# Kernel optimization log

Hardware: AMD Instinct MI355X
Metric: run time of the kernel (lower is better)

The kernel has to match this reference:

```python
import jax, jax.numpy as jnp
import numpy as np

D_MODEL = 1024
N_HEADS = 16
HEAD_DIM = D_MODEL // N_HEADS
D_FF = 4096
EPS = 1e-5


def layer_norm(x, w, b):
    mu = jnp.mean(x, axis=-1, keepdims=True)
    var = jnp.var(x, axis=-1, keepdims=True)
    return (x - mu) * jax.lax.rsqrt(var + EPS) * w + b


def setup_inputs() -> dict:
    key = jax.random.key(0)
    ks = jax.random.split(key, 8)
    B, T, C = 2, 2048, D_MODEL
    s = lambda fan_in: 1.0 / np.sqrt(fan_in)
    return {
        "x": jax.random.normal(ks[0], (B, T, C), dtype=jnp.float32),
        "ln1_w": jnp.ones((C,), jnp.float32),
        "ln1_b": jnp.zeros((C,), jnp.float32),
        "qkv_w": jax.random.normal(ks[1], (3 * C, C), jnp.float32) * s(C),
        "attn_out_w": jax.random.normal(ks[2], (C, C), jnp.float32) * s(C),
        "ln2_w": jnp.ones((C,), jnp.float32),
        "ln2_b": jnp.zeros((C,), jnp.float32),
        "mlp_in_w": jax.random.normal(ks[3], (D_FF, C), jnp.float32) * s(C),
        "mlp_gate_w": jax.random.normal(ks[4], (D_FF, C), jnp.float32) * s(C),
        "mlp_out_w": jax.random.normal(ks[5], (C, D_FF), jnp.float32) * s(D_FF),
    }


def reference(x, ln1_w, ln1_b, qkv_w, attn_out_w, ln2_w, ln2_b,
              mlp_in_w, mlp_gate_w, mlp_out_w):
    B, T, C = x.shape
    # --- causal self-attention (pre-norm) ---
    h = layer_norm(x, ln1_w, ln1_b)
    qkv = h @ qkv_w.T  # [B,T,3C]
    q, k, v = jnp.split(qkv, 3, axis=-1)
    def heads(t):
        return t.reshape(B, T, N_HEADS, HEAD_DIM).transpose(0, 2, 1, 3)  # [B,H,T,Dh]
    q, k, v = heads(q), heads(k), heads(v)
    scale = HEAD_DIM ** -0.5
    scores = jnp.einsum("bhqd,bhkd->bhqk", q, k) * scale  # [B,H,T,T]
    causal = jnp.tril(jnp.ones((T, T), dtype=bool))
    scores = jnp.where(causal, scores, -jnp.inf)
    attn = jax.nn.softmax(scores, axis=-1)
    out = jnp.einsum("bhqk,bhkd->bhqd", attn, v)
    out = out.transpose(0, 2, 1, 3).reshape(B, T, C)
    x = x + out @ attn_out_w.T
    # --- SwiGLU MLP (pre-norm) ---
    h = layer_norm(x, ln2_w, ln2_b)
    acts = jax.nn.silu(h @ mlp_in_w.T) * (h @ mlp_gate_w.T)
    return x + acts @ mlp_out_w.T
```

## Files before the change

kernel.cpp:

```cpp
#include <hip/hip_runtime.h>
#include <cstdint>

typedef unsigned short u16;
typedef __bf16 bf16x8 __attribute__((ext_vector_type(8)));
typedef float  f32x4  __attribute__((ext_vector_type(4)));

struct alignas(16) F4 { float v[4]; };
struct alignas(8)  U4 { u16 v[4]; };
struct alignas(16) U8 { u16 v[8]; };

__device__ __forceinline__ u16 f2bf(float f) {
    union { float f; unsigned int u; } x; x.f = f;
    unsigned int r = x.u + 0x7fffu + ((x.u >> 16) & 1u);
    return (u16)(r >> 16);
}
__device__ __forceinline__ float bf2f(u16 u) {
    union { unsigned int u; float f; } x; x.u = ((unsigned int)u) << 16;
    return x.f;
}
__device__ __forceinline__ f32x4 mfma16(bf16x8 a, bf16x8 b, f32x4 c) {
    return __builtin_amdgcn_mfma_f32_16x16x32_bf16(a, b, c, 0, 0, 0);
}
__device__ __forceinline__ bf16x8 ldf(const u16* p) { return *(const bf16x8*)p; }
__device__ __forceinline__ void gload_lds16(const void* g, void* l) {
    auto* gp = reinterpret_cast<const __attribute__((address_space(1))) unsigned int*>(
        reinterpret_cast<uintptr_t>(g));
    auto* lp = reinterpret_cast<__attribute__((address_space(3))) unsigned int*>(
        reinterpret_cast<uintptr_t>(l));
    __builtin_amdgcn_global_load_lds(gp, lp, 16, 0, 0);
}

__global__ __launch_bounds__(256) void cast_all_k(const float* __restrict__ qkvw,
                                                  const float* __restrict__ attow,
                                                  const float* __restrict__ mlpow,
                                                  const float* __restrict__ wi,
                                                  const float* __restrict__ wg,
                                                  u16* __restrict__ wq,
                                                  u16* __restrict__ wo,
                                                  u16* __restrict__ wm,
                                                  u16* __restrict__ wig) {
    constexpr int N1 = 3 * 1024 * 1024 / 8;
    constexpr int N2 = N1 + 1024 * 1024 / 8;
    constexpr int N3 = N2 + 1024 * 4096 / 8;
    const int i = blockIdx.x * 256 + threadIdx.x;
    const float* src; u16* dst;
    if (i < N1)      { src = qkvw  + (size_t)i * 8;        dst = wq + (size_t)i * 8; }
    else if (i < N2) { const int j = i - N1; src = attow + (size_t)j * 8; dst = wo + (size_t)j * 8; }
    else if (i < N3) { const int j = i - N2; src = mlpow + (size_t)j * 8; dst = wm + (size_t)j * 8; }
    else {
        const int j = i - N3;
        const int w = j >> 7, c8 = (j & 127) * 8;
        const int f = ((w >> 6) << 5) | (w & 31);
        src = ((w & 32) ? wg : wi) + (size_t)f * 1024 + c8;
        dst = wig + (size_t)w * 1024 + c8;
    }
    F4 a = *(const F4*)src;
    F4 b = *(const F4*)(src + 4);
    U8 o;
    #pragma unroll
    for (int j = 0; j < 4; ++j) { o.v[j] = f2bf(a.v[j]); o.v[4 + j] = f2bf(b.v[j]); }
    *(U8*)dst = o;
}

__global__ __launch_bounds__(256) void ln_fwd_k(const float* __restrict__ x,
                                                const float* __restrict__ w,
                                                const float* __restrict__ b,
                                                u16* __restrict__ h) {
    const int row = blockIdx.x, tid = threadIdx.x;
    const float* xr = x + (size_t)row * 1024;
    F4 v = *(const F4*)(xr + tid * 4);
    float s  = v.v[0] + v.v[1] + v.v[2] + v.v[3];
    float ss = v.v[0]*v.v[0] + v.v[1]*v.v[1] + v.v[2]*v.v[2] + v.v[3]*v.v[3];
    #pragma unroll
    for (int o = 32; o > 0; o >>= 1) { s += __shfl_down(s, o); ss += __shfl_down(ss, o); }
    __shared__ float red[8];
    const int wave = tid >> 6, lane = tid & 63;
    if (lane == 0) { red[wave] = s; red[4 + wave] = ss; }
    __syncthreads();
    s  = red[0] + red[1] + red[2] + red[3];
    ss = red[4] + red[5] + red[6] + red[7];
    const float mu   = s * (1.0f / 1024.0f);
    const float var  = ss * (1.0f / 1024.0f) - mu * mu;
    const float rstd = rsqrtf(var + 1e-5f);
    U4 o;
    #pragma unroll
    for (int j = 0; j < 4; ++j)
        o.v[j] = f2bf((v.v[j] - mu) * rstd * w[tid * 4 + j] + b[tid * 4 + j]);
    *(U4*)(h + (size_t)row * 1024 + tid * 4) = o;
}

__global__ __launch_bounds__(256) void ln_resid_k(const float* __restrict__ x,
                                                  const u16* __restrict__ p,
                                                  const float* __restrict__ w,
                                                  const float* __restrict__ b,
                                                  float* __restrict__ x1,
                                                  u16* __restrict__ h,
                                                  int planeEls) {
    const int row = blockIdx.x, tid = threadIdx.x;
    const size_t base = (size_t)row * 1024 + tid * 4;
    F4 xv = *(const F4*)(x + base);
    U4 q0 = *(const U4*)(p + base);
    U4 q1 = *(const U4*)(p + (size_t)planeEls + base);
    F4 sv;
    #pragma unroll
    for (int j = 0; j < 4; ++j) sv.v[j] = xv.v[j] + bf2f(q0.v[j]) + bf2f(q1.v[j]);
    *(F4*)(x1 + base) = sv;
    float s  = sv.v[0] + sv.v[1] + sv.v[2] + sv.v[3];
    float ss = sv.v[0]*sv.v[0] + sv.v[1]*sv.v[1] + sv.v[2]*sv.v[2] + sv.v[3]*sv.v[3];
    #pragma unroll
    for (int o = 32; o > 0; o >>= 1) { s += __shfl_down(s, o); ss += __shfl_down(ss, o); }
    __shared__ float red[8];
    const int wave = tid >> 6, lane = tid & 63;
    if (lane == 0) { red[wave] = s; red[4 + wave] = ss; }
    __syncthreads();
    s  = red[0] + red[1] + red[2] + red[3];
    ss = red[4] + red[5] + red[6] + red[7];
    const float mu   = s * (1.0f / 1024.0f);
    const float var  = ss * (1.0f / 1024.0f) - mu * mu;
    const float rstd = rsqrtf(var + 1e-5f);
    U4 o;
    #pragma unroll
    for (int j = 0; j < 4; ++j)
        o.v[j] = f2bf((sv.v[j] - mu) * rstd * w[tid * 4 + j] + b[tid * 4 + j]);
    *(U4*)(h + base) = o;
}

__global__ __launch_bounds__(256) void gemm_qkvt_k(const u16* __restrict__ h1,
                                                   const u16* __restrict__ wq,
                                                   u16* __restrict__ qk_b,
                                                   u16* __restrict__ vt_b) {
    __shared__ alignas(16) u16 Alds[128 * 32];
    __shared__ alignas(16) u16 Blds[128 * 32];
    const int tid  = threadIdx.x;
    const int lane = tid & 63, wave = tid >> 6;
    const int wr = wave >> 1, wc = wave & 1;
    const int r16 = lane & 15, g16 = lane >> 4;

    const u16* A; const u16* Bm; u16* Cout; int bn, bm, N;
    const int bid = blockIdx.x;
    if (bid < 512) { A = h1; Bm = wq; Cout = qk_b; N = 2048; bn = bid & 15; bm = bid >> 4; }
    else {
        const int id = bid - 512;
        A = wq + (size_t)2 * 1024 * 1024;
        Bm = h1; Cout = vt_b; N = 4096; bn = id & 31; bm = id >> 5;
    }
    constexpr int K = 1024;

    const int srow = lane >> 2;
    const int scol = (lane & 3) * 8;

    f32x4 acc[4][4] = {};

    for (int k0 = 0; k0 < K; k0 += 32) {
        #pragma unroll
        for (int c = 0; c < 2; ++c) {
            const int ch = wave * 2 + c;
            const u16* ga = A  + ((size_t)bm * 128 + ch * 16 + srow) * K + k0 + scol;
            gload_lds16(ga, &Alds[ch * 512]);
            const u16* gb = Bm + ((size_t)bn * 128 + ch * 16 + srow) * K + k0 + scol;
            gload_lds16(gb, &Blds[ch * 512]);
        }
        __syncthreads();
        bf16x8 af[4], bfr[4];
        #pragma unroll
        for (int m = 0; m < 4; ++m)
            af[m] = ldf(&Alds[(wr * 64 + m * 16 + r16) * 32 + g16 * 8]);
        #pragma unroll
        for (int n = 0; n < 4; ++n)
            bfr[n] = ldf(&Blds[(wc * 64 + n * 16 + r16) * 32 + g16 * 8]);
        #pragma unroll
        for (int m = 0; m < 4; ++m)
            #pragma unroll
            for (int n = 0; n < 4; ++n)
                acc[m][n] = mfma16(af[m], bfr[n], acc[m][n]);
        __syncthreads();
    }

    #pragma unroll
    for (int m = 0; m < 4; ++m)
        #pragma unroll
        for (int n = 0; n < 4; ++n)
            #pragma unroll
            for (int r = 0; r < 4; ++r) {
                const int row = bm * 128 + wr * 64 + m * 16 + g16 * 4 + r;
                const int col = bn * 128 + wc * 64 + n * 16 + r16;
                Cout[(size_t)row * N + col] = f2bf(acc[m][n][r]);
            }
}

__global__ __launch_bounds__(256) void gemm_btsplit_k(const u16* __restrict__ A,
                                                      const u16* __restrict__ Bm,
                                                      u16* __restrict__ P,
                                                      int N, int K, int kchunk,
                                                      int planeEls) {
    __shared__ alignas(16) u16 Alds[128 * 32];
    __shared__ alignas(16) u16 Blds[128 * 32];
    const int tid  = threadIdx.x;
    const int lane = tid & 63, wave = tid >> 6;
    const int wr = wave >> 1, wc = wave & 1;
    const int r16 = lane & 15, g16 = lane >> 4;
    const int bn = blockIdx.x, bm = blockIdx.y;
    const int kBeg = blockIdx.z * kchunk;

    const int srow = lane >> 2;
    const int scol = (lane & 3) * 8;

    f32x4 acc[4][4] = {};

    for (int k0 = kBeg; k0 < kBeg + kchunk; k0 += 32) {
        #pragma unroll
        for (int c = 0; c < 2; ++c) {
            const int ch = wave * 2 + c;
            const u16* ga = A  + ((size_t)bm * 128 + ch * 16 + srow) * K + k0 + scol;
            gload_lds16(ga, &Alds[ch * 512]);
            const u16* gb = Bm + ((size_t)bn * 128 + ch * 16 + srow) * K + k0 + scol;
            gload_lds16(gb, &Blds[ch * 512]);
        }
        __syncthreads();
        bf16x8 af[4], bfr[4];
        #pragma unroll
        for (int m = 0; m < 4; ++m)
            af[m] = ldf(&Alds[(wr * 64 + m * 16 + r16) * 32 + g16 * 8]);
        #pragma unroll
        for (int n = 0; n < 4; ++n)
            bfr[n] = ldf(&Blds[(wc * 64 + n * 16 + r16) * 32 + g16 * 8]);
        #pragma unroll
        for (int m = 0; m < 4; ++m)
            #pragma unroll
            for (int n = 0; n < 4; ++n)
                acc[m][n] = mfma16(af[m], bfr[n], acc[m][n]);
        __syncthreads();
    }

    u16* Pp = P + (size_t)blockIdx.z * planeEls;
    #pragma unroll
    for (int m = 0; m < 4; ++m)
        #pragma unroll
        for (int n = 0; n < 4; ++n)
            #pragma unroll
            for (int r = 0; r < 4; ++r) {
                const int row = bm * 128 + wr * 64 + m * 16 + g16 * 4 + r;
                const int col = bn * 128 + wc * 64 + n * 16 + r16;
                Pp[(size_t)row * N + col] = f2bf(acc[m][n][r]);
            }
}

template <int EPI>
__global__ __launch_bounds__(512, 2)
void gemm256_k(const u16* __restrict__ A, const u16* __restrict__ Bm,
               void* __restrict__ Cout, int lda, int ldb, int kLen,
               int nx, int bnCh, int outLd, int planeEls) {
    __shared__ alignas(16) u16 lds[2][2][2][128 * 64];

    const int tid  = threadIdx.x;
    const int wave = tid >> 6, lane = tid & 63;
    const int wm = wave >> 2, wn = wave & 3;
    const int r16 = lane & 15, g16 = lane >> 4;

    const int cpx = gridDim.x >> 3;
    const int xcd = blockIdx.x & 7, loc = blockIdx.x >> 3;
    const int mCh = cpx / bnCh;
    const int cpr = nx / bnCh;
    const int bm = (xcd / cpr) * mCh + loc / bnCh;
    const int bn = (xcd % cpr) * bnCh + loc % bnCh;
    const int kBeg = blockIdx.z * kLen;
    const int NT = kLen >> 6;

    const int csw = ((lane & 7) ^ (lane >> 3)) * 8;
    const u16* aU = A  + (size_t)(bm * 256) * lda + kBeg;
    const u16* bU = Bm + (size_t)(bn * 256) * ldb + kBeg;
    int aOff[2][2], bOff[2][2];
    #pragma unroll
    for (int h = 0; h < 2; ++h)
        #pragma unroll
        for (int i = 0; i < 2; ++i) {
            const int wr = wave * 16 + (lane >> 3) + i * 8;
            const int ar = (wr >> 6) * 128 + h * 64 + (wr & 63);
            const int br = (wr >> 5) * 64 + h * 32 + (wr & 31);
            aOff[h][i] = ar * lda + csw;
            bOff[h][i] = br * ldb + csw;
        }

    auto stA = [&](int kt, int h) {
        u16* d = &lds[kt & 1][0][h][wave * 1024];
        gload_lds16(aU + aOff[h][0] + kt * 64, d);
        gload_lds16(aU + aOff[h][1] + kt * 64, d + 512);
    };
    auto stB = [&](int kt, int h) {
        u16* d = &lds[kt & 1][1][h][wave * 1024];
        gload_lds16(bU + bOff[h][0] + kt * 64, d);
        gload_lds16(bU + bOff[h][1] + kt * 64, d + 512);
    };

    int offA[4][2], offB[2][2];
    #pragma unroll
    for (int m = 0; m < 4; ++m)
        #pragma unroll
        for (int ks = 0; ks < 2; ++ks)
            offA[m][ks] = (wm * 64 + m * 16 + r16) * 64 + (((ks * 4 + g16) ^ (r16 & 7)) * 8);
    #pragma unroll
    for (int n = 0; n < 2; ++n)
        #pragma unroll
        for (int ks = 0; ks < 2; ++ks)
            offB[n][ks] = (wn * 32 + n * 16 + r16) * 64 + (((ks * 4 + g16) ^ (r16 & 7)) * 8);

    f32x4 acc[8][4] = {};
    bf16x8 af0[4][2], af1[4][2], b0v[2][2], b1v[2][2];

    auto rdAF0 = [&](int buf) {
        const u16* P = &lds[buf][0][0][0];
        #pragma unroll
        for (int m = 0; m < 4; ++m) { af0[m][0] = ldf(P + offA[m][0]); af0[m][1] = ldf(P + offA[m][1]); }
    };
    auto rdAF1 = [&](int buf) {
        const u16* P = &lds[buf][0][1][0];
        #pragma unroll
        for (int m = 0; m < 4; ++m) { af1[m][0] = ldf(P + offA[m][0]); af1[m][1] = ldf(P + offA[m][1]); }
    };
    auto rdB0 = [&](int buf) {
        const u16* P = &lds[buf][1][0][0];
        #pragma unroll
        for (int n = 0; n < 2; ++n) { b0v[n][0] = ldf(P + offB[n][0]); b0v[n][1] = ldf(P + offB[n][1]); }
    };
    auto rdB1 = [&](int buf) {
        const u16* P = &lds[buf][1][1][0];
        #pragma unroll
        for (int n = 0; n < 2; ++n) { b1v[n][0] = ldf(P + offB[n][0]); b1v[n][1] = ldf(P + offB[n][1]); }
    };

    stA(0, 0); stB(0, 0); stB(0, 1); stA(0, 1);
    stA(1, 0); stB(1, 0); stB(1, 1); stA(1, 1);
    asm volatile("s_waitcnt vmcnt(8)" ::: "memory");
    __builtin_amdgcn_s_barrier();
    rdAF0(0); rdB0(0); rdB1(0); rdAF1(0);

    for (int kt = 0; kt < NT; ++kt) {
        const bool pf = (kt + 2 < NT);
        const int nb = (kt + 1) & 1;

        __builtin_amdgcn_s_setprio(1);
        #pragma unroll
        for (int m = 0; m < 4; ++m)
            #pragma unroll
            for (int n = 0; n < 2; ++n) {
                acc[m][n] = mfma16(af0[m][0], b0v[n][0], acc[m][n]);
                acc[m][n] = mfma16(af0[m][1], b0v[n][1], acc[m][n]);
            }
        __builtin_amdgcn_s_setprio(0);
        __builtin_amdgcn_s_barrier();

        if (pf) { stA(kt + 2, 0); stB(kt + 2, 0); }
        __builtin_amdgcn_s_setprio(1);
        #pragma unroll
        for (int m = 0; m < 4; ++m)
            #pragma unroll
            for (int n = 0; n < 2; ++n) {
                acc[m][n + 2] = mfma16(af0[m][0], b1v[n][0], acc[m][n + 2]);
                acc[m][n + 2] = mfma16(af0[m][1], b1v[n][1], acc[m][n + 2]);
            }
        __builtin_amdgcn_s_setprio(0);
        __builtin_amdgcn_s_barrier();

        if (pf) stB(kt + 2, 1);
        __builtin_amdgcn_s_setprio(1);
        #pragma unroll
        for (int m = 0; m < 4; ++m)
            #pragma unroll
            for (int n = 0; n < 2; ++n) {
                acc[m + 4][n] = mfma16(af1[m][0], b0v[n][0], acc[m + 4][n]);
                acc[m + 4][n] = mfma16(af1[m][1], b0v[n][1], acc[m + 4][n]);
            }
        __builtin_amdgcn_s_setprio(0);
        __builtin_amdgcn_s_barrier();

        if (pf) stA(kt + 2, 1);
        if (pf)               { asm volatile("s_waitcnt vmcnt(8)" ::: "memory"); }
        else if (kt + 1 < NT) { asm volatile("s_waitcnt vmcnt(0)" ::: "memory"); }
        if (kt + 1 < NT) {
            __builtin_amdgcn_s_barrier();
            rdAF0(nb); rdB0(nb);
        }
        __builtin_amdgcn_s_setprio(1);
        #pragma unroll
        for (int m = 0; m < 4; ++m)
            #pragma unroll
            for (int n = 0; n < 2; ++n) {
                acc[m + 4][n + 2] = mfma16(af1[m][0], b1v[n][0], acc[m + 4][n + 2]);
                acc[m + 4][n + 2] = mfma16(af1[m][1], b1v[n][1], acc[m + 4][n + 2]);
            }
        __builtin_amdgcn_s_setprio(0);
        if (kt + 1 < NT) { rdB1(nb); rdAF1(nb); }
    }

    if constexpr (EPI == 1) {
        u16* P = (u16*)Cout + (size_t)blockIdx.z * planeEls;
        #pragma unroll
        for (int m = 0; m < 8; ++m)
            #pragma unroll
            for (int n = 0; n < 4; ++n)
                #pragma unroll
                for (int r = 0; r < 4; ++r) {
                    const int row = bm * 256 + wm * 128 + m * 16 + g16 * 4 + r;
                    const int col = bn * 256 + wn * 64 + n * 16 + r16;
                    P[(size_t)row * outLd + col] = f2bf(acc[m][n][r]);
                }
    } else {
        (void)planeEls;
        u16* O = (u16*)Cout;
        #pragma unroll
        for (int m = 0; m < 8; ++m)
            #pragma unroll
            for (int n = 0; n < 2; ++n)
                #pragma unroll
                for (int r = 0; r < 4; ++r) {
                    const int row = bm * 256 + wm * 128 + m * 16 + g16 * 4 + r;
                    const int col = (bn * 4 + wn) * 32 + n * 16 + r16;
                    const float vi = acc[m][n][r];
                    const float vg = acc[m][n + 2][r];
                    const float sl = vi / (1.0f + __expf(-vi));
                    O[(size_t)row * outLd + col] = f2bf(sl * vg);
                }
    }
}

__global__ __launch_bounds__(256) void addreduce4_k(const float* __restrict__ resid,
                                                    const u16* __restrict__ p,
                                                    float* __restrict__ out,
                                                    int n4, int planeEls) {
    for (int i = blockIdx.x * 256 + threadIdx.x; i < n4; i += gridDim.x * 256) {
        F4 a = *(const F4*)(resid + (size_t)i * 4);
        U4 q0 = *(const U4*)(p + (size_t)i * 4);
        U4 q1 = *(const U4*)(p + (size_t)planeEls + (size_t)i * 4);
        U4 q2 = *(const U4*)(p + (size_t)2 * planeEls + (size_t)i * 4);
        U4 q3 = *(const U4*)(p + (size_t)3 * planeEls + (size_t)i * 4);
        F4 o;
        #pragma unroll
        for (int j = 0; j < 4; ++j)
            o.v[j] = a.v[j] + bf2f(q0.v[j]) + bf2f(q1.v[j]) + bf2f(q2.v[j]) + bf2f(q3.v[j]);
        *(F4*)(out + (size_t)i * 4) = o;
    }
}

__global__ __launch_bounds__(256) void attn_fwd_k(const u16* __restrict__ qk,
                                                  const u16* __restrict__ vt,
                                                  u16* __restrict__ Ob) {
    __shared__ alignas(16) u16 Klds[2][64 * 64];
    __shared__ alignas(16) u16 Vlds[2][64 * 64];

    const int tid  = threadIdx.x;
    const int wave = tid >> 6, lane = tid & 63;
    const int r16  = lane & 15, g16 = lane >> 4;

    const int blk = blockIdx.x;
    const int xcd = blk & 7;
    const int pc  = blk >> 3;
    const int hh  = pc >> 5;
    const int qb  = (31 - (pc & 31) + 8 * hh) & 31;
    const int bh  = xcd * 4 + hh;
    const int h   = bh & 15, b = bh >> 4;

    const int q0w = qb * 64 + wave * 16;
    const size_t seqb = (size_t)b * 2048;

    const u16* qp = qk + (seqb + q0w + r16) * 2048 + h * 64 + g16 * 8;
    const bf16x8 qf0 = *(const bf16x8*)qp;
    const bf16x8 qf1 = *(const bf16x8*)(qp + 32);

    const u16* kbase = qk + seqb * 2048 + 1024 + (size_t)h * 64;
    const u16* vbase = vt + (size_t)(h * 64) * 4096 + seqb;

    const int srow  = tid >> 3;
    const int scol8 = ((tid & 7) ^ (srow & 7)) * 8;
    const u16* ksrc = kbase + (size_t)srow * 2048 + scol8;
    const u16* vsrc = vbase + (size_t)srow * 4096 + scol8;

    auto stage = [&](int bufi, int kv0) {
        const u16* kp = ksrc + (size_t)kv0 * 2048;
        const u16* vp = vsrc + kv0;
        u16* kd = &Klds[bufi][wave * 512];
        u16* vd = &Vlds[bufi][wave * 512];
        gload_lds16(kp, kd);
        gload_lds16(kp + (size_t)32 * 2048, kd + 2048);
        gload_lds16(vp, vd);
        gload_lds16(vp + (size_t)32 * 4096, vd + 2048);
    };

    f32x4 o[4] = {};
    float mreg = -3.0e38f, lreg = 0.0f;
    constexpr float SC = 0.125f * 1.44269504088896341f;

    const int nt = qb + 1;
    stage(0, 0);
    asm volatile("s_waitcnt vmcnt(0)" ::: "memory");
    __builtin_amdgcn_s_barrier();

    for (int it = 0; it < nt; ++it) {
        const int kv0 = it * 64;
        const int cur = it & 1;
        if (it + 1 < nt) stage(cur ^ 1, kv0 + 64);

        const u16* K = Klds[cur];
        const u16* V = Vlds[cur];

        f32x4 s[4];
        #pragma unroll
        for (int t = 0; t < 4; ++t) {
            const int row = 16 * t + r16;
            const int sw  = row & 7;
            const bf16x8 k0 = *(const bf16x8*)&K[row * 64 + ((g16 ^ sw) * 8)];
            const bf16x8 k1 = *(const bf16x8*)&K[row * 64 + (((g16 + 4) ^ sw) * 8)];
            f32x4 acc = {0.f, 0.f, 0.f, 0.f};
            acc = mfma16(k0, qf0, acc);
            acc = mfma16(k1, qf1, acc);
            s[t] = acc;
        }

        float a[16];
        #pragma unroll
        for (int t = 0; t < 4; ++t)
            #pragma unroll
            for (int r = 0; r < 4; ++r) a[4 * t + r] = s[t][r] * SC;

        if (kv0 + 63 > q0w) {
            const int qg = q0w + r16;
            #pragma unroll
            for (int t = 0; t < 4; ++t)
                #pragma unroll
                for (int r = 0; r < 4; ++r)
                    if (kv0 + 16 * t + 4 * g16 + r > qg) a[4 * t + r] = -1.0e30f;
        }

        float mx = a[0];
        #pragma unroll
        for (int j = 1; j < 16; ++j) mx = fmaxf(mx, a[j]);
        mx = fmaxf(mx, __shfl_xor(mx, 16));
        mx = fmaxf(mx, __shfl_xor(mx, 32));
        const float mn = fmaxf(mreg, mx);
        const float al = exp2f(mreg - mn);
        float p[16], rs = 0.0f;
        #pragma unroll
        for (int j = 0; j < 16; ++j) { p[j] = exp2f(a[j] - mn); rs += p[j]; }
        rs += __shfl_xor(rs, 16);
        rs += __shfl_xor(rs, 32);
        lreg = lreg * al + rs;
        mreg = mn;

        bf16x8 pf0, pf1;
        #pragma unroll
        for (int j = 0; j < 8; ++j) { pf0[j] = (__bf16)p[j]; pf1[j] = (__bf16)p[8 + j]; }

        #pragma unroll
        for (int t = 0; t < 4; ++t) {
            const int row  = 16 * t + r16;
            const int sw   = row & 7;
            const int base = row * 64 + (g16 & 1) * 4;
            const int c0   = g16 >> 1;
            U4 a0 = *(const U4*)&V[base + (((c0 + 0) ^ sw) * 8)];
            U4 a1 = *(const U4*)&V[base + (((c0 + 2) ^ sw) * 8)];
            U4 b0 = *(const U4*)&V[base + (((c0 + 4) ^ sw) * 8)];
            U4 b1 = *(const U4*)&V[base + (((c0 + 6) ^ sw) * 8)];
            #pragma unroll
            for (int r = 0; r < 4; ++r) o[t][r] *= al;
            bf16x8 v0, v1;
            #pragma unroll
            for (int j = 0; j < 4; ++j) {
                v0[j]     = ((const __bf16*)&a0)[j];
                v0[4 + j] = ((const __bf16*)&a1)[j];
                v1[j]     = ((const __bf16*)&b0)[j];
                v1[4 + j] = ((const __bf16*)&b1)[j];
            }
            o[t] = mfma16(v0, pf0, o[t]);
            o[t] = mfma16(v1, pf1, o[t]);
        }

        if (it + 1 < nt) {
            asm volatile("s_waitcnt vmcnt(0)" ::: "memory");
            __builtin_amdgcn_s_barrier();
        }
    }

    const float inv = 1.0f / lreg;
    u16* op = Ob + (seqb + q0w + r16) * 1024 + h * 64 + 4 * g16;
    #pragma unroll
    for (int t = 0; t < 4; ++t) {
        U4 st;
        #pragma unroll
        for (int r = 0; r < 4; ++r) st.v[r] = f2bf(o[t][r] * inv);
        *(U4*)(op + 16 * t) = st;
    }
}

extern "C" void kernel_launch(void* const* d_in, const int* in_sizes, int n_in,
                              void* d_out, int out_size, void* d_ws, size_t ws_size,
                              hipStream_t stream) {
    (void)in_sizes; (void)n_in; (void)out_size; (void)ws_size;
    constexpr int C = 1024, FF = 4096, M = 2 * 2048;
    constexpr size_t MB = 1024 * 1024;

    const float* x      = (const float*)d_in[0];
    const float* ln1_w  = (const float*)d_in[1];
    const float* ln1_b  = (const float*)d_in[2];
    const float* qkv_w  = (const float*)d_in[3];
    const float* atto_w = (const float*)d_in[4];
    const float* ln2_w  = (const float*)d_in[5];
    const float* ln2_b  = (const float*)d_in[6];
    const float* mlpi_w = (const float*)d_in[7];
    const float* mlpg_w = (const float*)d_in[8];
    const float* mlpo_w = (const float*)d_in[9];
    float* out = (float*)d_out;

    char* ws = (char*)d_ws;
    size_t off = 0;
    auto alloc = [&](size_t bytes) {
        char* p = ws + off;
        off += (bytes + 255) & ~(size_t)255;
        return p;
    };
    u16*   wq   = (u16*)  alloc((size_t)3 * C * C * 2);
    u16*   wo   = (u16*)  alloc((size_t)C * C * 2);
    u16*   wig  = (u16*)  alloc((size_t)2 * FF * C * 2);
    u16*   wm   = (u16*)  alloc((size_t)C * FF * 2);
    float* x1   = (float*)alloc((size_t)M * C * 4);
    u16*   h2   = (u16*)  alloc((size_t)M * C * 2);
    u16*   ab   = (u16*)  alloc((size_t)M * FF * 2);
    char*  R    = alloc(64 * MB);
    u16*   h1   = (u16*)R;
    u16*   qk_b = (u16*)(R + 8 * MB);
    u16*   vt_b = (u16*)(R + 24 * MB);
    u16*   Ob   = (u16*)(R + 32 * MB);
    u16*   aoP  = (u16*)(R + 40 * MB);
    u16*   pscr = (u16*)R;

    cast_all_k<<<8192, 256, 0, stream>>>(qkv_w, atto_w, mlpo_w, mlpi_w, mlpg_w,
                                         wq, wo, wm, wig);

    ln_fwd_k<<<M, 256, 0, stream>>>(x, ln1_w, ln1_b, h1);
    gemm_qkvt_k<<<768, 256, 0, stream>>>(h1, wq, qk_b, vt_b);
    attn_fwd_k<<<1024, 256, 0, stream>>>(qk_b, vt_b, Ob);
    gemm_btsplit_k<<<dim3(C / 128, M / 128, 2), 256, 0, stream>>>(
        Ob, wo, aoP, C, C, C / 2, M * C);
    ln_resid_k<<<M, 256, 0, stream>>>(x, aoP, ln2_w, ln2_b, x1, h2, M * C);

    gemm256_k<2><<<dim3((2 * FF / 256) * (M / 256), 1, 1), 512, 0, stream>>>(
        h2, wig, ab, C, C, C, 2 * FF / 256, 8, FF, 0);
    gemm256_k<1><<<dim3((C / 256) * (M / 256), 1, 4), 512, 0, stream>>>(
        ab, wm, pscr, FF, FF, FF / 4, C / 256, 4, C, M * C);
    addreduce4_k<<<2048, 256, 0, stream>>>(x1, pscr, out, M * C / 4, M * C);
}
```

Baseline: 256.6 us.

## Fold softmax scale into Q, pre-permute V, pair causal blocks, skip rescale

The QKV GEMM epilogue now multiplies Q by the softmax scale times log2(e) and writes V^T columns in a permuted order. This lets the attention kernel drop the per-score multiply and load V fragments with two 16-byte LDS reads instead of four 8-byte reads plus repacking. The attention grid is halved so each block handles a long and a short causal query block (31-pi and pi), which balances work across blocks. The output rescale is skipped when no lane's running max grows. The risks are less parallelism from 512 blocks, loss of the earlier XCD-aware mapping, and a little extra precision loss from rounding Q to bf16 after scaling.

```diff
diff --git a/kernel.cpp b/kernel.cpp
--- a/kernel.cpp
+++ b/kernel.cpp
@@ -136,13 +136,13 @@
     const int wr = wave >> 1, wc = wave & 1;
     const int r16 = lane & 15, g16 = lane >> 4;
 
-    const u16* A; const u16* Bm; u16* Cout; int bn, bm, N;
+    const u16* A; const u16* Bm; u16* Cout; int bn, bm, N, role;
     const int bid = blockIdx.x;
-    if (bid < 512) { A = h1; Bm = wq; Cout = qk_b; N = 2048; bn = bid & 15; bm = bid >> 4; }
+    if (bid < 512) { A = h1; Bm = wq; Cout = qk_b; N = 2048; bn = bid & 15; bm = bid >> 4; role = 0; }
     else {
         const int id = bid - 512;
         A = wq + (size_t)2 * 1024 * 1024;
-        Bm = h1; Cout = vt_b; N = 4096; bn = id & 31; bm = id >> 5;
+        Bm = h1; Cout = vt_b; N = 4096; bn = id & 31; bm = id >> 5; role = 1;
     }
     constexpr int K = 1024;
 
@@ -176,6 +176,7 @@
         __syncthreads();
     }
 
+    constexpr float SCQ = 0.125f * 1.44269504088896341f;
     #pragma unroll
     for (int m = 0; m < 4; ++m)
         #pragma unroll
@@ -183,8 +184,16 @@
             #pragma unroll
             for (int r = 0; r < 4; ++r) {
                 const int row = bm * 128 + wr * 64 + m * 16 + g16 * 4 + r;
-                const int col = bn * 128 + wc * 64 + n * 16 + r16;
-                Cout[(size_t)row * N + col] = f2bf(acc[m][n][r]);
+                int col = bn * 128 + wc * 64 + n * 16 + r16;
+                float v = acc[m][n][r];
+                if (role == 0) {
+                    if (col < 1024) v *= SCQ;
+                } else {
+                    const int c5 = col & 31;
+                    const int pos = 8 * ((c5 & 15) >> 2) + 4 * (c5 >> 4) + (c5 & 3);
+                    col = (col & ~31) | pos;
+                }
+                Cout[(size_t)row * N + col] = f2bf(v);
             }
 }
 
@@ -451,20 +460,9 @@
     const int wave = tid >> 6, lane = tid & 63;
     const int r16  = lane & 15, g16 = lane >> 4;
 
-    const int blk = blockIdx.x;
-    const int xcd = blk & 7;
-    const int pc  = blk >> 3;
-    const int hh  = pc >> 5;
-    const int qb  = (31 - (pc & 31) + 8 * hh) & 31;
-    const int bh  = xcd * 4 + hh;
-    const int h   = bh & 15, b = bh >> 4;
-
-    const int q0w = qb * 64 + wave * 16;
+    const int bh = blockIdx.x >> 4, pi = blockIdx.x & 15;
+    const int h  = bh & 15, b = bh >> 4;
     const size_t seqb = (size_t)b * 2048;
-
-    const u16* qp = qk + (seqb + q0w + r16) * 2048 + h * 64 + g16 * 8;
-    const bf16x8 qf0 = *(const bf16x8*)qp;
-    const bf16x8 qf1 = *(const bf16x8*)(qp + 32);
 
     const u16* kbase = qk + seqb * 2048 + 1024 + (size_t)h * 64;
     const u16* vbase = vt + (size_t)(h * 64) * 4096 + seqb;
@@ -485,108 +483,114 @@
         gload_lds16(vp + (size_t)32 * 4096, vd + 2048);
     };
 
-    f32x4 o[4] = {};
-    float mreg = -3.0e38f, lreg = 0.0f;
-    constexpr float SC = 0.125f * 1.44269504088896341f;
-
-    const int nt = qb + 1;
-    stage(0, 0);
-    asm volatile("s_waitcnt vmcnt(0)" ::: "memory");
-    __builtin_amdgcn_s_barrier();
-
-    for (int it = 0; it < nt; ++it) {
-        const int kv0 = it * 64;
-        const int cur = it & 1;
-        if (it + 1 < nt) stage(cur ^ 1, kv0 + 64);
-
-        const u16* K = Klds[cur];
-        const u16* V = Vlds[cur];
-
-        f32x4 s[4];
-        #pragma unroll
-        for (int t = 0; t < 4; ++t) {
-            const int row = 16 * t + r16;
-            const int sw  = row & 7;
-            const bf16x8 k0 = *(const bf16x8*)&K[row * 64 + ((g16 ^ sw) * 8)];
-            const bf16x8 k1 = *(const bf16x8*)&K[row * 64 + (((g16 + 4) ^ sw) * 8)];
-            f32x4 acc = {0.f, 0.f, 0.f, 0.f};
-            acc = mfma16(k0, qf0, acc);
-            acc = mfma16(k1, qf1, acc);
-            s[t] = acc;
-        }
-
-        float a[16];
-        #pragma unroll
-        for (int t = 0; t < 4; ++t)
-            #pragma unroll
-            for (int r = 0; r < 4; ++r) a[4 * t + r] = s[t][r] * SC;
-
-        if (kv0 + 63 > q0w) {
-            const int qg = q0w + r16;
+    #pragma unroll 1
+    for (int half = 0; half < 2; ++half) {
+        const int qb  = half ? pi : (31 - pi);
+        const int q0w = qb * 64 + wave * 16;
+
+        const u16* qp = qk + (seqb + q0w + r16) * 2048 + h * 64 + g16 * 8;
+        const bf16x8 qf0 = *(const bf16x8*)qp;
+        const bf16x8 qf1 = *(const bf16x8*)(qp + 32);
+
+        f32x4 o[4] = {};
+        float mreg = -3.0e38f, lreg = 0.0f;
+        const int nt = qb + 1;
+
+        if (half) __syncthreads();
+        stage(0, 0);
+        asm volatile("s_waitcnt vmcnt(0)" ::: "memory");
+        __builtin_amdgcn_s_barrier();
+
+        for (int it = 0; it < nt; ++it) {
+            const int kv0 = it * 64;
+            const int cur = it & 1;
+            if (it + 1 < nt) stage(cur ^ 1, kv0 + 64);
+
+            const u16* K = Klds[cur];
+            const u16* V = Vlds[cur];
+
+            f32x4 s[4];
+            #pragma unroll
+            for (int t = 0; t < 4; ++t) {
+                const int row = 16 * t + r16;
+                const int sw  = row & 7;
+                const bf16x8 k0 = ldf(&K[row * 64 + ((g16 ^ sw) * 8)]);
+                const bf16x8 k1 = ldf(&K[row * 64 + (((g16 + 4) ^ sw) * 8)]);
+                f32x4 acc = {0.f, 0.f, 0.f, 0.f};
+                acc = mfma16(k0, qf0, acc);
+                acc = mfma16(k1, qf1, acc);
+                s[t] = acc;
+            }
+
+            float a[16];
             #pragma unroll
             for (int t = 0; t < 4; ++t)
                 #pragma unroll
-                for (int r = 0; r < 4; ++r)
-                    if (kv0 + 16 * t + 4 * g16 + r > qg) a[4 * t + r] = -1.0e30f;
+                for (int r = 0; r < 4; ++r) a[4 * t + r] = s[t][r];
+
+            if (kv0 + 63 > q0w) {
+                const int qg = q0w + r16;
+                #pragma unroll
+                for (int t = 0; t < 4; ++t)
+                    #pragma unroll
+                    for (int r = 0; r < 4; ++r)
+                        if (kv0 + 16 * t + 4 * g16 + r > qg) a[4 * t + r] = -1.0e30f;
+            }
+
+            float mx = a[0];
+            #pragma unroll
+            for (int j = 1; j < 16; ++j) mx = fmaxf(mx, a[j]);
+            mx = fmaxf(mx, __shfl_xor(mx, 16));
+            mx = fmaxf(mx, __shfl_xor(mx, 32));
+
+            const float mn = fmaxf(mreg, mx);
+            float p[16], rs = 0.0f;
+            #pragma unroll
+            for (int j = 0; j < 16; ++j) { p[j] = exp2f(a[j] - mn); rs += p[j]; }
+            rs += __shfl_xor(rs, 16);
+            rs += __shfl_xor(rs, 32);
+
+            if (__all(mx <= mreg)) {
+                lreg += rs;
+            } else {
+                const float al = exp2f(mreg - mn);
+                lreg = lreg * al + rs;
+                mreg = mn;
+                #pragma unroll
+                for (int t = 0; t < 4; ++t)
+                    #pragma unroll
+                    for (int r = 0; r < 4; ++r) o[t][r] *= al;
+            }
+
+            bf16x8 pf0, pf1;
+            #pragma unroll
+            for (int j = 0; j < 8; ++j) { pf0[j] = (__bf16)p[j]; pf1[j] = (__bf16)p[8 + j]; }
+
+            #pragma unroll
+            for (int t = 0; t < 4; ++t) {
+                const int row = 16 * t + r16;
+                const int sw  = row & 7;
+                const bf16x8 v0 = ldf(&V[row * 64 + ((g16 ^ sw) * 8)]);
+                const bf16x8 v1 = ldf(&V[row * 64 + (((4 + g16) ^ sw) * 8)]);
+                o[t] = mfma16(v0, pf0, o[t]);
+                o[t] = mfma16(v1, pf1, o[t]);
+            }
+
+            if (it + 1 < nt) {
+                asm volatile("s_waitcnt vmcnt(0)" ::: "memory");
+                __builtin_amdgcn_s_barrier();
+            }
         }
 
-        float mx = a[0];
-        #pragma unroll
-        for (int j = 1; j < 16; ++j) mx = fmaxf(mx, a[j]);
-        mx = fmaxf(mx, __shfl_xor(mx, 16));
-        mx = fmaxf(mx, __shfl_xor(mx, 32));
-        const float mn = fmaxf(mreg, mx);
-        const float al = exp2f(mreg - mn);
-        float p[16], rs = 0.0f;
-        #pragma unroll
-        for (int j = 0; j < 16; ++j) { p[j] = exp2f(a[j] - mn); rs += p[j]; }
-        rs += __shfl_xor(rs, 16);
-        rs += __shfl_xor(rs, 32);
-        lreg = lreg * al + rs;
-        mreg = mn;
-
-        bf16x8 pf0, pf1;
-        #pragma unroll
-        for (int j = 0; j < 8; ++j) { pf0[j] = (__bf16)p[j]; pf1[j] = (__bf16)p[8 + j]; }
-
+        const float inv = 1.0f / lreg;
+        u16* op = Ob + (seqb + q0w + r16) * 1024 + h * 64 + 4 * g16;
         #pragma unroll
         for (int t = 0; t < 4; ++t) {
-            const int row  = 16 * t + r16;
-            const int sw   = row & 7;
-            const int base = row * 64 + (g16 & 1) * 4;
-            const int c0   = g16 >> 1;
-            U4 a0 = *(const U4*)&V[base + (((c0 + 0) ^ sw) * 8)];
-            U4 a1 = *(const U4*)&V[base + (((c0 + 2) ^ sw) * 8)];
-            U4 b0 = *(const U4*)&V[base + (((c0 + 4) ^ sw) * 8)];
-            U4 b1 = *(const U4*)&V[base + (((c0 + 6) ^ sw) * 8)];
-            #pragma unroll
-            for (int r = 0; r < 4; ++r) o[t][r] *= al;
-            bf16x8 v0, v1;
-            #pragma unroll
-            for (int j = 0; j < 4; ++j) {
-                v0[j]     = ((const __bf16*)&a0)[j];
-                v0[4 + j] = ((const __bf16*)&a1)[j];
-                v1[j]     = ((const __bf16*)&b0)[j];
-                v1[4 + j] = ((const __bf16*)&b1)[j];
-            }
-            o[t] = mfma16(v0, pf0, o[t]);
-            o[t] = mfma16(v1, pf1, o[t]);
+            U4 st;
+            #pragma unroll
+            for (int r = 0; r < 4; ++r) st.v[r] = f2bf(o[t][r] * inv);
+            *(U4*)(op + 16 * t) = st;
         }
-
-        if (it + 1 < nt) {
-            asm volatile("s_waitcnt vmcnt(0)" ::: "memory");
-            __builtin_amdgcn_s_barrier();
-        }
-    }
-
-    const float inv = 1.0f / lreg;
-    u16* op = Ob + (seqb + q0w + r16) * 1024 + h * 64 + 4 * g16;
-    #pragma unroll
-    for (int t = 0; t < 4; ++t) {
-        U4 st;
-        #pragma unroll
-        for (int r = 0; r < 4; ++r) st.v[r] = f2bf(o[t][r] * inv);
-        *(U4*)(op + 16 * t) = st;
     }
 }
 
@@ -636,7 +640,7 @@
 
     ln_fwd_k<<<M, 256, 0, stream>>>(x, ln1_w, ln1_b, h1);
     gemm_qkvt_k<<<768, 256, 0, stream>>>(h1, wq, qk_b, vt_b);
-    attn_fwd_k<<<1024, 256, 0, stream>>>(qk_b, vt_b, Ob);
+    attn_fwd_k<<<512, 256, 0, stream>>>(qk_b, vt_b, Ob);
     gemm_btsplit_k<<<dim3(C / 128, M / 128, 2), 256, 0, stream>>>(
         Ob, wo, aoP, C, C, C / 2, M * C);
     ln_resid_k<<<M, 256, 0, stream>>>(x, aoP, ln2_w, ln2_b, x1, h2, M * C);
```

Result: faster. 244.1 us (median of 3 runs) (-4.9%).
